# Kernel tuning notes

Measured on AMD Instinct MI355X. Metric: run time of the kernel, lower is better.

The kernel has to match this reference:

```python
import jax, jax.numpy as jnp
import numpy as np

HIDDEN = 2048
N_HEADS = 16
N_KV_HEADS = 4
HEAD_DIM = HIDDEN // N_HEADS  # 128
ROPE_THETA = 10000.0


def setup_inputs() -> dict:
    key = jax.random.key(0)
    ks = jax.random.split(key, 5)
    B, S = 2, 2048
    scale = 0.02
    return {
        "hidden_states": jax.random.normal(ks[0], (B, S, HIDDEN), jnp.float32),
        "Wq": jax.random.normal(ks[1], (HIDDEN, N_HEADS * HEAD_DIM), jnp.float32) * scale,
        "Wk": jax.random.normal(ks[2], (HIDDEN, N_KV_HEADS * HEAD_DIM), jnp.float32) * scale,
        "Wv": jax.random.normal(ks[3], (HIDDEN, N_KV_HEADS * HEAD_DIM), jnp.float32) * scale,
        "Wo": jax.random.normal(ks[4], (HIDDEN, HIDDEN), jnp.float32) * scale,
    }


def _rope_tables(seq_len, dim, dtype):
    inv_freq = 1.0 / (ROPE_THETA ** (jnp.arange(0, dim, 2, dtype=jnp.float32) / dim))
    t = jnp.arange(seq_len, dtype=jnp.float32)
    freqs = jnp.outer(t, inv_freq)            # [S, dim/2]
    emb = jnp.concatenate([freqs, freqs], -1)  # [S, dim]
    return jnp.cos(emb).astype(dtype), jnp.sin(emb).astype(dtype)


def _rotate_half(x):
    d = x.shape[-1] // 2
    return jnp.concatenate([-x[..., d:], x[..., :d]], axis=-1)


def _mqa_forward(hidden_states, Wq, Wk, Wv, Wo):
    B, S, _ = hidden_states.shape
    q = (hidden_states @ Wq).reshape(B, S, N_HEADS, HEAD_DIM).transpose(0, 2, 1, 3)      # [B,H,S,D]
    k = (hidden_states @ Wk).reshape(B, S, N_KV_HEADS, HEAD_DIM).transpose(0, 2, 1, 3)   # [B,Hkv,S,D]
    v = (hidden_states @ Wv).reshape(B, S, N_KV_HEADS, HEAD_DIM).transpose(0, 2, 1, 3)

    cos, sin = _rope_tables(S, HEAD_DIM, q.dtype)  # [S,D]
    q = q * cos + _rotate_half(q) * sin
    k = k * cos + _rotate_half(k) * sin

    # GQA: group query heads over shared KV heads instead of repeat_kv (same math)
    g = N_HEADS // N_KV_HEADS
    qg = q.reshape(B, N_KV_HEADS, g, S, HEAD_DIM)
    scale = 1.0 / np.sqrt(HEAD_DIM)
    scores = jnp.einsum("bhgqd,bhkd->bhgqk", qg, k) * scale  # [B,Hkv,g,S,S]
    causal = jnp.tril(jnp.ones((S, S), bool))
    scores = jnp.where(causal, scores, -jnp.inf)
    probs = jax.nn.softmax(scores.astype(jnp.float32), axis=-1).astype(q.dtype)
    out = jnp.einsum("bhgqk,bhkd->bhgqd", probs, v)  # [B,Hkv,g,S,D]
    out = out.reshape(B, N_HEADS, S, HEAD_DIM).transpose(0, 2, 1, 3).reshape(B, S, HIDDEN)
    return out @ Wo


def reference(hidden_states, Wq, Wk, Wv, Wo):
    return _mqa_forward(hidden_states, Wq, Wk, Wv, Wo)
```

## Files before the change

### kernel.cpp

```cpp
#include <hip/hip_runtime.h>
#include <hip/hip_bf16.h>
#include <cstdint>
#include <cstddef>

#define HIDDEN   2048
#define NH       16
#define NKV      4
#define HD       128
#define SEQ      2048
#define BATCH    2
#define NTOK     (BATCH*SEQ)
#define QKV_LD   3072
#define KOFF     2048
#define VOFF     2560
#define SM_SCALE 0.08838834764831845f
#define LOG2E    1.4426950408889634f

typedef __attribute__((ext_vector_type(8)))  short bf16x8;
typedef __attribute__((ext_vector_type(4)))  float f32x4v;
typedef __attribute__((ext_vector_type(16))) float f32x16;
typedef unsigned short ushort_t;

__device__ __forceinline__ unsigned short f2bf(float f) {
  return __builtin_bit_cast(unsigned short, __float2bfloat16(f));
}
__device__ __forceinline__ float bf2f(ushort_t u) {
  return __builtin_bit_cast(float, (unsigned)u << 16);
}
__device__ __forceinline__ unsigned pack2(float a, float b) {
  return (unsigned)f2bf(a) | ((unsigned)f2bf(b) << 16);
}

__device__ __forceinline__ void gload16(const void* g, void* l) {
  __builtin_amdgcn_global_load_lds(
      (const __attribute__((address_space(1))) unsigned int*)g,
      (__attribute__((address_space(3))) unsigned int*)l, 16, 0, 0);
}

__global__ __launch_bounds__(256) void conv_f2b(
    const float* __restrict__ in, ushort_t* __restrict__ out, int n8)
{
  const int i = blockIdx.x*256 + threadIdx.x;
  if (i >= n8) return;
  const float4 a = ((const float4*)in)[2*i];
  const float4 b = ((const float4*)in)[2*i + 1];
  uint4 r;
  r.x = pack2(a.x, a.y); r.y = pack2(a.z, a.w);
  r.z = pack2(b.x, b.y); r.w = pack2(b.z, b.w);
  ((uint4*)out)[i] = r;
}

__global__ __launch_bounds__(256) void transpose_f2b(
    const float* __restrict__ W, ushort_t* __restrict__ Wt, int K, int N)
{
  __shared__ float tile[32][33];
  const int n0 = blockIdx.x*32, k0 = blockIdx.y*32;
  const int tx = threadIdx.x & 31, ty = threadIdx.x >> 5;
  #pragma unroll
  for (int i = 0; i < 4; ++i)
    tile[ty*4 + i][tx] = W[(size_t)(k0 + ty*4 + i)*N + n0 + tx];
  __syncthreads();
  #pragma unroll
  for (int i = 0; i < 4; ++i) {
    const int nl = ty*4 + i;
    Wt[(size_t)(n0 + nl)*K + k0 + tx] = f2bf(tile[tx][nl]);
  }
}

template<bool B16OUT>
__global__ __launch_bounds__(256) void bt_gemm(
    const ushort_t* __restrict__ A, const ushort_t* __restrict__ Bt,
    void* __restrict__ Cv, int ldc)
{
  __shared__ ushort_t As[128*64];
  __shared__ ushort_t Bs[128*64];
  const int t = threadIdx.x, lane = t & 63, w = t >> 6;
  const int bm = blockIdx.y*128, bn = blockIdx.x*128;
  const int wr = w >> 1, wc = w & 1;
  const int lr = lane & 15, lg = lane >> 4;

  f32x4v acc[4][4];
  #pragma unroll
  for (int fm = 0; fm < 4; ++fm)
    #pragma unroll
    for (int fn = 0; fn < 4; ++fn)
      #pragma unroll
      for (int r = 0; r < 4; ++r) acc[fm][fn][r] = 0.f;

  const char* Ab = (const char*)A;
  const char* Bb = (const char*)Bt;
  char* asb = (char*)As;
  char* bsb = (char*)Bs;

  for (int kt = 0; kt < HIDDEN*2; kt += 128) {
    __syncthreads();
    #pragma unroll
    for (int u = 0; u < 4; ++u) {
      const int idx = u*256 + t;
      const int row = idx >> 3;
      const int kb  = (idx & 7) * 16;
      const int skb = kb ^ ((row & 7) << 4);
      gload16(Ab + (size_t)(bm + row)*4096 + kt + skb, asb + idx*16);
      gload16(Bb + (size_t)(bn + row)*4096 + kt + skb, bsb + idx*16);
    }
    __syncthreads();
    #pragma unroll
    for (int kc = 0; kc < 2; ++kc) {
      bf16x8 af[4], bfr[4];
      #pragma unroll
      for (int f = 0; f < 4; ++f) {
        const int rm = wr*64 + f*16 + lr;
        af[f]  = *(const bf16x8*)(asb + rm*128 + ((kc*64 + lg*16) ^ ((rm & 7) << 4)));
        const int rn = wc*64 + f*16 + lr;
        bfr[f] = *(const bf16x8*)(bsb + rn*128 + ((kc*64 + lg*16) ^ ((rn & 7) << 4)));
      }
      #pragma unroll
      for (int fm = 0; fm < 4; ++fm)
        #pragma unroll
        for (int fn = 0; fn < 4; ++fn)
          acc[fm][fn] = __builtin_amdgcn_mfma_f32_16x16x32_bf16(af[fm], bfr[fn], acc[fm][fn], 0, 0, 0);
    }
  }

  #pragma unroll
  for (int fm = 0; fm < 4; ++fm) {
    const int m = bm + wr*64 + fm*16 + lg*4;
    #pragma unroll
    for (int fn = 0; fn < 4; ++fn) {
      const int n = bn + wc*64 + fn*16 + lr;
      #pragma unroll
      for (int r = 0; r < 4; ++r) {
        if constexpr (B16OUT)
          ((ushort_t*)Cv)[(size_t)(m + r)*ldc + n] = f2bf(acc[fm][fn][r]);
        else
          ((float*)Cv)[(size_t)(m + r)*ldc + n] = acc[fm][fn][r];
      }
    }
  }
}

__global__ __launch_bounds__(256) void rope_conv(
    const ushort_t* __restrict__ QKVb, ushort_t* __restrict__ Qo,
    ushort_t* __restrict__ Ko)
{
  const int total = NTOK * (NH + NKV) * (HD/2);
  int idx = blockIdx.x * 256 + threadIdx.x;
  if (idx >= total) return;
  const int i   = idx & 63;
  int tmp = idx >> 6;
  const int hs  = tmp % (NH + NKV);
  const int tkn = tmp / (NH + NKV);
  const int s   = tkn & (SEQ - 1);
  const int b   = tkn >> 11;
  const float invf = expf(-(float)i * 0.14391156831212787f);
  float sn, cs;
  sincosf((float)s * invf, &sn, &cs);
  const size_t base = (size_t)tkn * QKV_LD + (hs < NH ? hs * HD : KOFF + (hs - NH) * HD);
  const float x0 = bf2f(QKVb[base + i]);
  const float x1 = bf2f(QKVb[base + i + 64]);
  const float y0 = x0 * cs - x1 * sn;
  const float y1 = x1 * cs + x0 * sn;
  if (hs < NH) {
    ushort_t* q = Qo + (size_t)tkn * HIDDEN + hs * HD;
    q[i]      = f2bf(y0 * (SM_SCALE * LOG2E));
    q[i + 64] = f2bf(y1 * (SM_SCALE * LOG2E));
  } else {
    ushort_t* k = Ko + ((size_t)(b*NKV + (hs - NH))*SEQ + s) * HD;
    k[i]      = f2bf(y0);
    k[i + 64] = f2bf(y1);
  }
}

__global__ __launch_bounds__(256) void vt_conv(
    const ushort_t* __restrict__ QKVb, ushort_t* __restrict__ Vtb)
{
  __shared__ ushort_t tile[32][33];
  const int s0 = blockIdx.x*32;
  const int d0 = (blockIdx.y & 3)*32;
  const int bk = blockIdx.y >> 2;
  const int b = bk >> 2, hk = bk & 3;
  const int tx = threadIdx.x & 31, ty = threadIdx.x >> 5;
  #pragma unroll
  for (int i = 0; i < 4; ++i) {
    const int sl = ty*4 + i;
    tile[sl][tx] = QKVb[(size_t)(b*SEQ + s0 + sl)*QKV_LD + VOFF + hk*HD + d0 + tx];
  }
  __syncthreads();
  #pragma unroll
  for (int i = 0; i < 4; ++i) {
    const int dl = ty*4 + i;
    Vtb[((size_t)bk*HD + d0 + dl)*SEQ + s0 + tx] = tile[tx][dl];
  }
}

__global__ __launch_bounds__(256) void attn_mfma7(
    const ushort_t* __restrict__ Qb, const ushort_t* __restrict__ Kb,
    const ushort_t* __restrict__ Vtb, ushort_t* __restrict__ O)
{
  __shared__ char smem[49152];

  const int bx = blockIdx.x;
  const int qt = 63 - (int)blockIdx.y;
  const int b = bx >> 2, hk = bx & 3;
  const int t = threadIdx.x, w = t >> 6, lane = t & 63;
  const int c = lane & 31, hi = lane >> 5;
  const int h = hk*4 + w;
  const int qw0 = qt*32;
  const int qg  = qw0 + c;
  const int nsteps = (qt + 2) >> 1;

  const char* Kbb = (const char*)(Kb + (size_t)(b*NKV + hk)*SEQ*HD);
  const char* Vbb = (const char*)(Vtb + (size_t)(b*NKV + hk)*HD*SEQ);
  char* klds = smem;
  char* vlds = smem + 16384;
  char* plb  = smem + 32768 + w*4096;

  int ksrc[4], vsrc[4], ldst[4];
  #pragma unroll
  for (int u = 0; u < 4; ++u) {
    const int idx = u*256 + t;
    const int krow = idx >> 4, kof = (idx & 15) << 4;
    ksrc[u] = krow*256 + (kof ^ ((krow & 15) << 4));
    const int vd = idx >> 3,  vof = (idx & 7) << 4;
    vsrc[u] = vd*(SEQ*2) + (vof ^ ((vd & 7) << 4));
    ldst[u] = idx*16;
  }

  bf16x8 qf[8];
  {
    const ushort_t* qrow = Qb + (size_t)(b*SEQ + qg)*HIDDEN + h*HD;
    #pragma unroll
    for (int kc = 0; kc < 8; ++kc)
      qf[kc] = *(const bf16x8*)(qrow + kc*16 + hi*8);
  }

  f32x16 ot[4];
  #pragma unroll
  for (int nc = 0; nc < 4; ++nc)
    #pragma unroll
    for (int r = 0; r < 16; ++r) ot[nc][r] = 0.f;
  float m = -1e30f, l = 0.f;

  #pragma unroll
  for (int u = 0; u < 4; ++u) {
    gload16(Kbb + ksrc[u], klds + ldst[u]);
    gload16(Vbb + vsrc[u], vlds + ldst[u]);
  }
  __syncthreads();

  for (int kt = 0; kt < nsteps; ++kt) {
    f32x16 s[2];
    #pragma unroll
    for (int kn = 0; kn < 2; ++kn)
      #pragma unroll
      for (int r = 0; r < 16; ++r) s[kn][r] = 0.f;
    #pragma unroll
    for (int kn = 0; kn < 2; ++kn) {
      const int row = kn*32 + c;
      const int sw = (row & 15) << 4;
      #pragma unroll
      for (int kc = 0; kc < 8; ++kc) {
        const bf16x8 ka = *(const bf16x8*)(klds + row*256 + ((kc*32 + hi*16) ^ sw));
        s[kn] = __builtin_amdgcn_mfma_f32_32x32x16_bf16(ka, qf[kc], s[kn], 0, 0, 0);
      }
    }
    if (kt == nsteps - 1) {
      #pragma unroll
      for (int kn = 0; kn < 2; ++kn)
        #pragma unroll
        for (int r = 0; r < 16; ++r) {
          const int kg_ = kt*64 + kn*32 + (r & 3) + 8*(r >> 2) + 4*hi;
          if (kg_ > qg) s[kn][r] = -1e30f;
        }
    }
    float mx[16];
    #pragma unroll
    for (int r = 0; r < 16; ++r) mx[r] = fmaxf(s[0][r], s[1][r]);
    #pragma unroll
    for (int st = 8; st > 0; st >>= 1)
      #pragma unroll
      for (int r = 0; r < 8; ++r)
        if (r < st) mx[r] = fmaxf(mx[r], mx[r + st]);
    const float pm = fmaxf(mx[0], __shfl_xor(mx[0], 32));
    if (!__all(pm - m <= 8.f)) {
      const float mnew = fmaxf(m, pm);
      const float corr = exp2f(m - mnew);
      m = mnew;
      l *= corr;
      #pragma unroll
      for (int nc = 0; nc < 4; ++nc) ot[nc] *= corr;
    }
    float ls = 0.f;
    #pragma unroll
    for (int kn = 0; kn < 2; ++kn)
      #pragma unroll
      for (int r = 0; r < 16; ++r) {
        const float p = exp2f(s[kn][r] - m);
        ls += p;
        s[kn][r] = p;
      }
    l += ls;
    {
      const int swp = (c & 7) << 4;
      #pragma unroll
      for (int kn = 0; kn < 2; ++kn)
        #pragma unroll
        for (int r = 0; r < 16; r += 2) {
          const int key = kn*32 + (r & 3) + 8*(r >> 2) + 4*hi;
          *(unsigned*)(plb + c*128 + ((key*2) ^ swp)) = pack2(s[kn][r], s[kn][r+1]);
        }
    }
    asm volatile("s_waitcnt lgkmcnt(0)" ::: "memory");
    #pragma unroll
    for (int kc = 0; kc < 4; ++kc) {
      const bf16x8 pb = *(const bf16x8*)(plb + c*128 + ((kc*32 + hi*16) ^ ((c & 7) << 4)));
      #pragma unroll
      for (int nc = 0; nc < 4; ++nc) {
        const int dim = nc*32 + c;
        const bf16x8 va = *(const bf16x8*)(vlds + dim*128 + ((kc*32 + hi*16) ^ ((dim & 7) << 4)));
        ot[nc] = __builtin_amdgcn_mfma_f32_32x32x16_bf16(va, pb, ot[nc], 0, 0, 0);
      }
    }
    if (kt < nsteps - 1) {
      __syncthreads();
      const size_t kto = (size_t)(kt + 1) * 16384;
      const int    vto = (kt + 1) * 128;
      #pragma unroll
      for (int u = 0; u < 4; ++u) {
        gload16(Kbb + kto + ksrc[u], klds + ldst[u]);
        gload16(Vbb + vto + vsrc[u], vlds + ldst[u]);
      }
      __syncthreads();
    }
  }

  const float lt = l + __shfl_xor(l, 32);
  const float inv = 1.f / lt;
  ushort_t* orow = O + (size_t)(b*SEQ + qg) * HIDDEN + h*HD;
  #pragma unroll
  for (int nc = 0; nc < 4; ++nc)
    #pragma unroll
    for (int r = 0; r < 16; r += 2) {
      const int dim = nc*32 + (r & 3) + 8*(r >> 2) + 4*hi;
      *(unsigned*)(orow + dim) = pack2(ot[nc][r]*inv, ot[nc][r+1]*inv);
    }
}

extern "C" void kernel_launch(void* const* d_in, const int* in_sizes, int n_in,
                              void* d_out, int out_size, void* d_ws, size_t ws_size,
                              hipStream_t stream)
{
  (void)in_sizes; (void)n_in; (void)out_size; (void)ws_size;
  const float* H  = (const float*)d_in[0];
  const float* Wq = (const float*)d_in[1];
  const float* Wk = (const float*)d_in[2];
  const float* Wv = (const float*)d_in[3];
  const float* Wo = (const float*)d_in[4];
  float* out = (float*)d_out;

  char* ws = (char*)d_ws;
  ushort_t* QKVb = (ushort_t*)ws;
  ushort_t* Hb   = (ushort_t*)(ws + 25165824);
  ushort_t* Qb   = Hb;
  ushort_t* Wt   = (ushort_t*)(ws + 41943040);
  ushort_t* Kb   = (ushort_t*)(ws + 54525952);
  ushort_t* Vtb  = (ushort_t*)(ws + 58720256);
  ushort_t* Oat  = (ushort_t*)(ws + 62914560);

  conv_f2b<<<4096, 256, 0, stream>>>(H, Hb, NTOK*HIDDEN/8);
  transpose_f2b<<<dim3(64, 64), 256, 0, stream>>>(Wq, Wt,                     2048, 2048);
  transpose_f2b<<<dim3(16, 64), 256, 0, stream>>>(Wk, Wt + (size_t)2048*2048, 2048, 512);
  transpose_f2b<<<dim3(16, 64), 256, 0, stream>>>(Wv, Wt + (size_t)2560*2048, 2048, 512);

  bt_gemm<true><<<dim3(QKV_LD/128, NTOK/128), 256, 0, stream>>>(Hb, Wt, QKVb, QKV_LD);

  const int rope_total = NTOK * (NH + NKV) * (HD/2);
  rope_conv<<<(rope_total + 255)/256, 256, 0, stream>>>(QKVb, Qb, Kb);
  vt_conv<<<dim3(SEQ/32, 32), 256, 0, stream>>>(QKVb, Vtb);

  attn_mfma7<<<dim3(8, 64), 256, 0, stream>>>(Qb, Kb, Vtb, Oat);

  transpose_f2b<<<dim3(64, 64), 256, 0, stream>>>(Wo, Wt, 2048, 2048);
  bt_gemm<false><<<dim3(HIDDEN/128, NTOK/128), 256, 0, stream>>>(Oat, Wt, out, HIDDEN);
}
```

Measured before the change: 247.5 us.

## Split long causal query tiles across two blocks and merge; remap GEMM block order

The attention kernel now splits the 32 longest query tiles' KV range into two halves handled by separate blocks. Each half writes an unnormalized partial output plus running max and sum, and a new merge kernel combines the pairs. This gives 768 blocks instead of 512 and evens out causal load imbalance, at the cost of extra partial-output traffic and one more launch. The GEMM also remaps block IDs into a strided order, likely to improve cache locality or spread work across XCDs.

```diff
diff --git a/kernel.cpp b/kernel.cpp
--- a/kernel.cpp
+++ b/kernel.cpp
@@ -75,7 +75,11 @@
   __shared__ ushort_t As[128*64];
   __shared__ ushort_t Bs[128*64];
   const int t = threadIdx.x, lane = t & 63, w = t >> 6;
-  const int bm = blockIdx.y*128, bn = blockIdx.x*128;
+  const int gx = gridDim.x;
+  const int d  = blockIdx.y*gx + blockIdx.x;
+  const int qc = (gx*gridDim.y) >> 3;
+  const int sid = (d & 7)*qc + (d >> 3);
+  const int bm = (sid / gx)*128, bn = (sid % gx)*128;
   const int wr = w >> 1, wc = w & 1;
   const int lr = lane & 15, lg = lane >> 4;
 
@@ -193,14 +197,18 @@
   }
 }
 
-__global__ __launch_bounds__(256) void attn_mfma7(
+__global__ __launch_bounds__(256) void attn_mfma8(
     const ushort_t* __restrict__ Qb, const ushort_t* __restrict__ Kb,
-    const ushort_t* __restrict__ Vtb, ushort_t* __restrict__ O)
+    const ushort_t* __restrict__ Vtb, ushort_t* __restrict__ O,
+    ushort_t* __restrict__ Po, float2* __restrict__ ML)
 {
   __shared__ char smem[49152];
 
   const int bx = blockIdx.x;
-  const int qt = 63 - (int)blockIdx.y;
+  const int y  = blockIdx.y;
+  int qt, chunk; bool dual;
+  if (y < 64) { qt = 63 - (y >> 1); chunk = y & 1; dual = true; }
+  else        { qt = 95 - y;        chunk = 0;     dual = false; }
   const int b = bx >> 2, hk = bx & 3;
   const int t = threadIdx.x, w = t >> 6, lane = t & 63;
   const int c = lane & 31, hi = lane >> 5;
@@ -208,6 +216,9 @@
   const int qw0 = qt*32;
   const int qg  = qw0 + c;
   const int nsteps = (qt + 2) >> 1;
+  const int half = (nsteps + 1) >> 1;
+  const int k0 = (dual && chunk == 1) ? half : 0;
+  const int k1 = (dual && chunk == 0) ? half : nsteps;
 
   const char* Kbb = (const char*)(Kb + (size_t)(b*NKV + hk)*SEQ*HD);
   const char* Vbb = (const char*)(Vtb + (size_t)(b*NKV + hk)*HD*SEQ);
@@ -241,14 +252,18 @@
     for (int r = 0; r < 16; ++r) ot[nc][r] = 0.f;
   float m = -1e30f, l = 0.f;
 
-  #pragma unroll
-  for (int u = 0; u < 4; ++u) {
-    gload16(Kbb + ksrc[u], klds + ldst[u]);
-    gload16(Vbb + vsrc[u], vlds + ldst[u]);
+  {
+    const size_t kto = (size_t)k0 * 16384;
+    const int    vto = k0 * 128;
+    #pragma unroll
+    for (int u = 0; u < 4; ++u) {
+      gload16(Kbb + kto + ksrc[u], klds + ldst[u]);
+      gload16(Vbb + vto + vsrc[u], vlds + ldst[u]);
+    }
   }
   __syncthreads();
 
-  for (int kt = 0; kt < nsteps; ++kt) {
+  for (int kt = k0; kt < k1; ++kt) {
     f32x16 s[2];
     #pragma unroll
     for (int kn = 0; kn < 2; ++kn)
@@ -321,7 +336,7 @@
         ot[nc] = __builtin_amdgcn_mfma_f32_32x32x16_bf16(va, pb, ot[nc], 0, 0, 0);
       }
     }
-    if (kt < nsteps - 1) {
+    if (kt < k1 - 1) {
       __syncthreads();
       const size_t kto = (size_t)(kt + 1) * 16384;
       const int    vto = (kt + 1) * 128;
@@ -335,15 +350,49 @@
   }
 
   const float lt = l + __shfl_xor(l, 32);
-  const float inv = 1.f / lt;
-  ushort_t* orow = O + (size_t)(b*SEQ + qg) * HIDDEN + h*HD;
-  #pragma unroll
-  for (int nc = 0; nc < 4; ++nc)
-    #pragma unroll
-    for (int r = 0; r < 16; r += 2) {
-      const int dim = nc*32 + (r & 3) + 8*(r >> 2) + 4*hi;
-      *(unsigned*)(orow + dim) = pack2(ot[nc][r]*inv, ot[nc][r+1]*inv);
-    }
+  if (!dual) {
+    const float inv = 1.f / lt;
+    ushort_t* orow = O + (size_t)(b*SEQ + qg) * HIDDEN + h*HD;
+    #pragma unroll
+    for (int nc = 0; nc < 4; ++nc)
+      #pragma unroll
+      for (int r = 0; r < 16; r += 2) {
+        const int dim = nc*32 + (r & 3) + 8*(r >> 2) + 4*hi;
+        *(unsigned*)(orow + dim) = pack2(ot[nc][r]*inv, ot[nc][r+1]*inv);
+      }
+  } else {
+    const int rec = (((qt - 32)*8 + bx)*4 + w)*32 + c + chunk*32768;
+    ushort_t* orow = Po + (size_t)rec * 128;
+    #pragma unroll
+    for (int nc = 0; nc < 4; ++nc)
+      #pragma unroll
+      for (int r = 0; r < 16; r += 2) {
+        const int dim = nc*32 + (r & 3) + 8*(r >> 2) + 4*hi;
+        *(unsigned*)(orow + dim) = pack2(ot[nc][r], ot[nc][r+1]);
+      }
+    if (hi == 0) ML[rec] = make_float2(m, lt);
+  }
+}
+
+__global__ __launch_bounds__(256) void merge_attn(
+    const ushort_t* __restrict__ Po, const float2* __restrict__ ML,
+    ushort_t* __restrict__ Oat)
+{
+  const int rec  = blockIdx.x*4 + (threadIdx.x >> 6);
+  const int lane = threadIdx.x & 63;
+  const float2 ml0 = ML[rec], ml1 = ML[rec + 32768];
+  const float ms = fmaxf(ml0.x, ml1.x);
+  const float w0 = exp2f(ml0.x - ms), w1 = exp2f(ml1.x - ms);
+  const float inv = 1.f / (ml0.y*w0 + ml1.y*w1);
+  const int c  = rec & 31, wv = (rec >> 5) & 3, bx = (rec >> 7) & 7, qt = 32 + (rec >> 10);
+  const int b = bx >> 2, hk = bx & 3, hh = hk*4 + wv;
+  const ushort_t* p0 = Po + (size_t)rec * 128;
+  const ushort_t* p1 = p0 + (size_t)32768 * 128;
+  ushort_t* dst = Oat + (size_t)(b*SEQ + qt*32 + c)*HIDDEN + hh*HD;
+  const int d = lane*2;
+  const float a0 = bf2f(p0[d]), a1 = bf2f(p0[d+1]);
+  const float b0 = bf2f(p1[d]), b1 = bf2f(p1[d+1]);
+  *(unsigned*)(dst + d) = pack2((a0*w0 + b0*w1)*inv, (a1*w0 + b1*w1)*inv);
 }
 
 extern "C" void kernel_launch(void* const* d_in, const int* in_sizes, int n_in,
@@ -366,6 +415,8 @@
   ushort_t* Kb   = (ushort_t*)(ws + 54525952);
   ushort_t* Vtb  = (ushort_t*)(ws + 58720256);
   ushort_t* Oat  = (ushort_t*)(ws + 62914560);
+  ushort_t* Po   = (ushort_t*)ws;
+  float2*   ML   = (float2*)(ws + 16777216);
 
   conv_f2b<<<4096, 256, 0, stream>>>(H, Hb, NTOK*HIDDEN/8);
   transpose_f2b<<<dim3(64, 64), 256, 0, stream>>>(Wq, Wt,                     2048, 2048);
@@ -378,7 +429,8 @@
   rope_conv<<<(rope_total + 255)/256, 256, 0, stream>>>(QKVb, Qb, Kb);
   vt_conv<<<dim3(SEQ/32, 32), 256, 0, stream>>>(QKVb, Vtb);
 
-  attn_mfma7<<<dim3(8, 64), 256, 0, stream>>>(Qb, Kb, Vtb, Oat);
+  attn_mfma8<<<dim3(8, 96), 256, 0, stream>>>(Qb, Kb, Vtb, Oat, Po, ML);
+  merge_attn<<<8192, 256, 0, stream>>>(Po, ML, Oat);
 
   transpose_f2b<<<dim3(64, 64), 256, 0, stream>>>(Wo, Wt, 2048, 2048);
   bt_gemm<false><<<dim3(HIDDEN/128, NTOK/128), 256, 0, stream>>>(Oat, Wt, out, HIDDEN);
```

After: 269.6 us. 8.9% more time.
